# Kernel optimization log

Measured on AMD Instinct MI355X. Metric: run time of the kernel, lower is better.

## Reference

```python
import jax, jax.numpy as jnp
import numpy as np

BN_EPS = 1e-5

def _square_distance(src, dst):
    # src [B,N,3], dst [B,S,3] -> [B,N,S]
    d = -2.0 * jnp.einsum('bnc,bsc->bns', src, dst)
    d = d + jnp.sum(src * src, -1)[:, :, None]
    d = d + jnp.sum(dst * dst, -1)[:, None, :]
    return d

def _conv_bn_relu(x, w, b, g, beta):
    # x [B,C,N]; 1x1 conv == channel GEMM, then training-mode batchnorm over (B,N)
    y = jnp.einsum('oc,bcn->bon', w, x) + b[None, :, None]
    mean = jnp.mean(y, axis=(0, 2), keepdims=True)
    var = jnp.mean((y - mean) ** 2, axis=(0, 2), keepdims=True)  # biased, as torch BN uses for normalization
    y = (y - mean) * jax.lax.rsqrt(var + BN_EPS)
    y = y * g[None, :, None] + beta[None, :, None]
    return jax.nn.relu(y)

def setup_inputs() -> dict:
    key = jax.random.key(0)
    ks = jax.random.split(key, 8)
    B, N, S, D1, D2 = 8, 8192, 2048, 128, 256
    C_in, C_mid, C_out = D1 + D2, 256, 256
    return {
        'xyz1': jax.random.normal(ks[0], (B, 3, N), jnp.float32),
        'xyz2': jax.random.normal(ks[1], (B, 3, S), jnp.float32),
        'points1': jax.random.normal(ks[2], (B, D1, N), jnp.float32),
        'points2': jax.random.normal(ks[3], (B, D2, S), jnp.float32),
        'w1': jax.random.normal(ks[4], (C_mid, C_in), jnp.float32) * (1.0 / np.sqrt(C_in)),
        'b1': jax.random.normal(ks[5], (C_mid,), jnp.float32) * 0.01,
        'g1': jnp.ones((C_mid,), jnp.float32),
        'beta1': jnp.zeros((C_mid,), jnp.float32),
        'w2': jax.random.normal(ks[6], (C_out, C_mid), jnp.float32) * (1.0 / np.sqrt(C_mid)),
        'b2': jax.random.normal(ks[7], (C_out,), jnp.float32) * 0.01,
        'g2': jnp.ones((C_out,), jnp.float32),
        'beta2': jnp.zeros((C_out,), jnp.float32),
    }

def reference(xyz1, xyz2, points1, points2, w1, b1, g1, beta1, w2, b2, g2, beta2):
    B = xyz1.shape[0]
    p1xyz = jnp.transpose(xyz1, (0, 2, 1))      # [B,N,3]
    p2xyz = jnp.transpose(xyz2, (0, 2, 1))      # [B,S,3]
    p2 = jnp.transpose(points2, (0, 2, 1))      # [B,S,D2]

    dists = _square_distance(p1xyz, p2xyz)      # [B,N,S]
    neg_d3, idx = jax.lax.top_k(-dists, 3)      # 3 smallest distances
    d3 = -neg_d3                                # [B,N,3]
    recip = 1.0 / (d3 + 1e-8)
    weight = recip / jnp.sum(recip, axis=2, keepdims=True)  # [B,N,3]

    gathered = jax.vmap(lambda p, i: p[i])(p2, idx)          # [B,N,3,D2]
    interp = jnp.sum(gathered * weight[..., None], axis=2)   # [B,N,D2]

    new_points = jnp.concatenate([jnp.transpose(points1, (0, 2, 1)), interp], axis=-1)
    x = jnp.transpose(new_points, (0, 2, 1))    # [B,D1+D2,N]
    x = _conv_bn_relu(x, w1, b1, g1, beta1)
    x = _conv_bn_relu(x, w2, b2, g2, beta2)
    return x
```

## Files before the change

### kernel.cpp

```cpp
#include <hip/hip_runtime.h>

#define B_    8
#define N_    8192
#define S_    2048
#define D1_   128
#define D2_   256
#define CIN_  384
#define CMID_ 256
#define COUT_ 256

typedef unsigned int  u32;
typedef unsigned short u16;
typedef __attribute__((ext_vector_type(8))) short short8;
typedef __attribute__((ext_vector_type(4))) float f32x4;

static __device__ __forceinline__ u32 uminu(u32 a, u32 b) { return a < b ? a : b; }
static __device__ __forceinline__ u32 umaxu(u32 a, u32 b) { return a > b ? a : b; }
static __device__ __forceinline__ u32 umed3(u32 a, u32 b, u32 c) {
  u32 d;
  asm("v_med3_u32 %0, %1, %2, %3" : "=v"(d) : "v"(a), "v"(b), "v"(c));
  return d;
}
static __device__ __forceinline__ u16 f2bf(float f) {
  union { float f; u32 u; } v; v.f = f;
  u32 r = v.u + 0x7FFFu + ((v.u >> 16) & 1u);
  return (u16)(r >> 16);
}
static __device__ __forceinline__ float bflo(u32 u) { return __uint_as_float(u << 16); }
static __device__ __forceinline__ float bfhi(u32 u) { return __uint_as_float(u & 0xFFFF0000u); }
static __device__ __forceinline__ u32 cvtpk_bf16(float lo, float hi) {
  u32 d;
  asm("v_cvt_pk_bf16_f32 %0, %1, %2" : "=v"(d) : "v"(lo), "v"(hi));
  return d;
}

#define GLD16(g, l)                                                             \
  __builtin_amdgcn_global_load_lds((const __attribute__((address_space(1))) void*)(g), \
                                   (__attribute__((address_space(3))) void*)(l), 16, 0, 0)

__global__ __launch_bounds__(256) void k_pre(const float* __restrict__ xyz2,
                                             float4* __restrict__ pts4,
                                             const float* __restrict__ w1,
                                             const float* __restrict__ w2,
                                             u16* __restrict__ w1b,
                                             u16* __restrict__ w2b) {
  const int i = blockIdx.x * 256 + threadIdx.x;
  if (i < B_ * S_) {
    const int b = i >> 11, s = i & (S_ - 1);
    const float* xb = xyz2 + (size_t)b * 3 * S_;
    float x = xb[s], y = xb[S_ + s], z = xb[2 * S_ + s];
    pts4[b * S_ + s] = make_float4(-2.f * x, -2.f * y, -2.f * z, x * x + y * y + z * z);
    return;
  }
  const int j = i - B_ * S_;
  if (j < CMID_ * CIN_) { w1b[j] = f2bf(w1[j]); return; }
  const int h = j - CMID_ * CIN_;
  if (h < COUT_ * CMID_) w2b[h] = f2bf(w2[h]);
}

__global__ __launch_bounds__(256) void k_nn_scan(const float* __restrict__ xyz1,
                                                 const float4* __restrict__ pts4,
                                                 uint4* __restrict__ keys) {
  const int b = blockIdx.z, chunk = blockIdx.y;
  const int n = blockIdx.x * 256 + threadIdx.x;
  const float* pb = xyz1 + (size_t)b * 3 * N_;
  const float px = pb[n], py = pb[N_ + n], pz = pb[2 * N_ + n];
  const float pn = px * px + py * py + pz * pz;
  const float4* __restrict__ P = pts4 + b * S_ + chunk * 256;
  u32 m0 = ~0u, m1 = ~0u, m2 = ~0u;
#pragma unroll 8
  for (int s = 0; s < 256; ++s) {
    float4 q = P[s];
    float d = fmaf(px, q.x, fmaf(py, q.y, fmaf(pz, q.z, pn + q.w)));
    d = fmaxf(d, 0.f);
    u32 k = (__float_as_uint(d) & 0xFFFFFF00u) | (u32)s;
    u32 t = umaxu(m1, k);
    m1 = umed3(m0, m1, k);
    m2 = uminu(m2, t);
    m0 = uminu(m0, k);
  }
  uint4 v; v.x = m0; v.y = m1; v.z = m2; v.w = m2;
  keys[((size_t)(b * 8 + chunk)) * N_ + n] = v;
}

__global__ __launch_bounds__(256) void k_refine(const float* __restrict__ xyz1,
                                                const float4* __restrict__ pts4,
                                                const uint4* __restrict__ keys,
                                                int4* __restrict__ idx4,
                                                float4* __restrict__ w4) {
  const int b = blockIdx.y, n = blockIdx.x * 256 + threadIdx.x;
  const float* pb = xyz1 + (size_t)b * 3 * N_;
  const double px = (double)pb[n], py = (double)pb[N_ + n], pz = (double)pb[2 * N_ + n];
  const double pn = px * px + py * py + pz * pz;
  double bd0 = 1e300, bd1 = 1e300, bd2 = 1e300;
  int bi0 = 1 << 30, bi1 = 1 << 30, bi2 = 1 << 30;
#pragma unroll
  for (int c = 0; c < 8; ++c) {
    uint4 kk = keys[((size_t)(b * 8 + c)) * N_ + n];
    u32 arr[3] = {kk.x, kk.y, kk.z};
#pragma unroll
    for (int j = 0; j < 3; ++j) {
      int s = c * 256 + (int)(arr[j] & 255u);
      float4 q = pts4[b * S_ + s];
      double x = (double)(q.x * -0.5f), y = (double)(q.y * -0.5f), z = (double)(q.z * -0.5f);
      double dot = px * x + py * y + pz * z;
      double d = -2.0 * dot + (pn + (x * x + y * y + z * z));
      if (d < bd2 || (d == bd2 && s < bi2)) {
        if (d < bd1 || (d == bd1 && s < bi1)) {
          bd2 = bd1; bi2 = bi1;
          if (d < bd0 || (d == bd0 && s < bi0)) { bd1 = bd0; bi1 = bi0; bd0 = d; bi0 = s; }
          else                                  { bd1 = d;  bi1 = s; }
        } else { bd2 = d; bi2 = s; }
      }
    }
  }
  float f0 = (float)bd0, f1 = (float)bd1, f2 = (float)bd2;
  float r0 = 1.f / (f0 + 1e-8f), r1 = 1.f / (f1 + 1e-8f), r2 = 1.f / (f2 + 1e-8f);
  float rs = r0 + r1 + r2;
  w4[(size_t)b * N_ + n]   = make_float4(r0 / rs, r1 / rs, r2 / rs, 0.f);
  idx4[(size_t)b * N_ + n] = make_int4(bi0, bi1, bi2, 0);
}

__global__ __launch_bounds__(256) void k_p2t(const float* __restrict__ p2,
                                             float* __restrict__ p2T) {
  __shared__ float t[32][33];
  const int b = blockIdx.z, s0 = blockIdx.x * 32, d0 = blockIdx.y * 32;
  const int cc = threadIdx.x & 31, rr = threadIdx.x >> 5;
#pragma unroll
  for (int i = 0; i < 4; ++i) {
    int r = rr + i * 8;
    t[r][cc] = p2[((size_t)b * D2_ + d0 + r) * S_ + s0 + cc];
  }
  __syncthreads();
#pragma unroll
  for (int i = 0; i < 4; ++i) {
    int r = rr + i * 8;
    p2T[((size_t)b * S_ + s0 + r) * D2_ + d0 + cc] = t[cc][r];
  }
}

__global__ __launch_bounds__(256) void k_packp1(const float* __restrict__ p1,
                                                u16* __restrict__ xT) {
  __shared__ float t[32][33];
  const int b = blockIdx.z, n0 = blockIdx.x * 32, c0 = blockIdx.y * 32;
  const int cc = threadIdx.x & 31, rr = threadIdx.x >> 5;
#pragma unroll
  for (int i = 0; i < 4; ++i) {
    int r = rr + i * 8;
    t[r][cc] = p1[((size_t)b * D1_ + c0 + r) * N_ + n0 + cc];
  }
  __syncthreads();
#pragma unroll
  for (int i = 0; i < 4; ++i) {
    int r = rr + i * 8;
    xT[((size_t)b * N_ + n0 + r) * CIN_ + c0 + cc] = f2bf(t[cc][r]);
  }
}

__global__ __launch_bounds__(256) void k_gather_pack(const float* __restrict__ p2T,
                                                     const int4* __restrict__ idx4,
                                                     const float4* __restrict__ w4,
                                                     u16* __restrict__ xT) {
  const int b = blockIdx.y;
  const int wv = threadIdx.x >> 6, lane = threadIdx.x & 63;
  const int nbase = blockIdx.x * 16 + wv * 4;
  int4   id[4];
  float4 w[4];
#pragma unroll
  for (int i = 0; i < 4; ++i) {
    id[i] = idx4[(size_t)b * N_ + nbase + i];
    w[i]  = w4[(size_t)b * N_ + nbase + i];
  }
#pragma unroll
  for (int i = 0; i < 4; ++i) {
    const int n = nbase + i;
    const float4* r0 = (const float4*)(p2T + ((size_t)b * S_ + id[i].x) * D2_) + lane;
    const float4* r1 = (const float4*)(p2T + ((size_t)b * S_ + id[i].y) * D2_) + lane;
    const float4* r2 = (const float4*)(p2T + ((size_t)b * S_ + id[i].z) * D2_) + lane;
    float4 a = *r0, bb = *r1, cq = *r2;
    ushort4 pk;
    pk.x = f2bf(a.x * w[i].x + bb.x * w[i].y + cq.x * w[i].z);
    pk.y = f2bf(a.y * w[i].x + bb.y * w[i].y + cq.y * w[i].z);
    pk.z = f2bf(a.z * w[i].x + bb.z * w[i].y + cq.z * w[i].z);
    pk.w = f2bf(a.w * w[i].x + bb.w * w[i].y + cq.w * w[i].z);
    *(ushort4*)(xT + ((size_t)b * N_ + n) * CIN_ + D1_ + lane * 4) = pk;
  }
}

__global__ __launch_bounds__(64) void k_bnstat(const float* __restrict__ ps,
                                               const float* __restrict__ pq,
                                               const float* __restrict__ g,
                                               const float* __restrict__ beta,
                                               float* __restrict__ scale,
                                               float* __restrict__ shift) {
  const int o = blockIdx.x, l = threadIdx.x;
  float s = 0.f, q = 0.f;
#pragma unroll
  for (int i = 0; i < 8; ++i) {
    s += ps[(size_t)o * 512 + i * 64 + l];
    q += pq[(size_t)o * 512 + i * 64 + l];
  }
#pragma unroll
  for (int m = 1; m <= 32; m <<= 1) { s += __shfl_xor(s, m); q += __shfl_xor(q, m); }
  if (l == 0) {
    const float inv = 1.0f / (float)(B_ * N_);
    float mean = s * inv;
    float var = q * inv - mean * mean;
    float sc = g[o] / sqrtf(var + 1e-5f);
    scale[o] = sc;
    shift[o] = beta[o] - mean * sc;
  }
}

__global__ __launch_bounds__(512) void k_gemm1(const u16* __restrict__ Wb,
                                               const float* __restrict__ bias,
                                               const u16* __restrict__ xT,
                                               u16* __restrict__ y1T,
                                               float* __restrict__ psum,
                                               float* __restrict__ pssq) {
  __shared__ u16 As[2][8192];
  __shared__ u16 Bs[2][4096];
  __shared__ float s_sum[256], s_ssq[256];
  const int b = blockIdx.z, bn0 = blockIdx.x * 128;
  const int tid = threadIdx.x, w = tid >> 6, l = tid & 63;
  const int wm = w & 3, wn = w >> 2;
  const int lr = l >> 2, lc = l & 3;
  const int fm = l & 15, fq = l >> 4;
  const int clog = (lc ^ ((lr >> 1) & 3)) * 8;
  const int swz8 = (fq ^ ((fm >> 1) & 3)) * 8;
  if (tid < 256) { s_sum[tid] = 0.f; s_ssq[tid] = 0.f; }
  f32x4 acc[4][4];
#pragma unroll
  for (int i = 0; i < 4; ++i)
#pragma unroll
    for (int j = 0; j < 4; ++j) acc[i][j] = (f32x4){0.f, 0.f, 0.f, 0.f};

  const int NK = CIN_ / 32;
#pragma unroll
  for (int j = 0; j < 2; ++j) {
    int seg = w * 2 + j, row = seg * 16 + lr;
    GLD16(Wb + (size_t)row * CIN_ + clog, &As[0][seg * 512]);
  }
  {
    int row = w * 16 + lr;
    GLD16(xT + ((size_t)b * N_ + bn0 + row) * CIN_ + clog, &Bs[0][w * 512]);
  }
  for (int kk = 0; kk < NK; ++kk) {
    __syncthreads();
    const int cur = kk & 1;
    if (kk + 1 < NK) {
      const int k0 = (kk + 1) * 32, nxt = cur ^ 1;
#pragma unroll
      for (int j = 0; j < 2; ++j) {
        int seg = w * 2 + j, row = seg * 16 + lr;
        GLD16(Wb + (size_t)row * CIN_ + k0 + clog, &As[nxt][seg * 512]);
      }
      int row = w * 16 + lr;
      GLD16(xT + ((size_t)b * N_ + bn0 + row) * CIN_ + k0 + clog, &Bs[nxt][w * 512]);
    }
    short8 af[4], bfr[4];
#pragma unroll
    for (int f = 0; f < 4; ++f) {
      af[f]  = *(const short8*)&As[cur][(wm * 64 + f * 16 + fm) * 32 + swz8];
      bfr[f] = *(const short8*)&Bs[cur][(wn * 64 + f * 16 + fm) * 32 + swz8];
    }
#pragma unroll
    for (int i = 0; i < 4; ++i)
#pragma unroll
      for (int j = 0; j < 4; ++j)
        acc[i][j] = __builtin_amdgcn_mfma_f32_16x16x32_bf16(af[i], bfr[j], acc[i][j], 0, 0, 0);
  }
  u16* tb = y1T + ((size_t)b * 64 + (bn0 >> 7)) * 32768;
#pragma unroll
  for (int i = 0; i < 4; ++i) {
    int ob = wm * 64 + i * 16 + fq * 4;
    float4 b4 = *(const float4*)(bias + ob);
    float sv0 = 0, sv1 = 0, sv2 = 0, sv3 = 0, qv0 = 0, qv1 = 0, qv2 = 0, qv3 = 0;
#pragma unroll
    for (int j = 0; j < 4; ++j) {
      int nl = wn * 64 + j * 16 + fm;
      ushort4 pk;
      pk.x = f2bf(acc[i][j][0] + b4.x);
      pk.y = f2bf(acc[i][j][1] + b4.y);
      pk.z = f2bf(acc[i][j][2] + b4.z);
      pk.w = f2bf(acc[i][j][3] + b4.w);
      *(ushort4*)(tb + (size_t)(ob >> 5) * 4096 + nl * 32 + (ob & 31)) = pk;
      float v0 = bflo(pk.x), v1 = bflo(pk.y), v2 = bflo(pk.z), v3 = bflo(pk.w);
      sv0 += v0; sv1 += v1; sv2 += v2; sv3 += v3;
      qv0 = fmaf(v0, v0, qv0); qv1 = fmaf(v1, v1, qv1);
      qv2 = fmaf(v2, v2, qv2); qv3 = fmaf(v3, v3, qv3);
    }
#pragma unroll
    for (int m = 1; m <= 8; m <<= 1) {
      sv0 += __shfl_xor(sv0, m); sv1 += __shfl_xor(sv1, m);
      sv2 += __shfl_xor(sv2, m); sv3 += __shfl_xor(sv3, m);
      qv0 += __shfl_xor(qv0, m); qv1 += __shfl_xor(qv1, m);
      qv2 += __shfl_xor(qv2, m); qv3 += __shfl_xor(qv3, m);
    }
    if (fm == 0) {
      atomicAdd(&s_sum[ob + 0], sv0); atomicAdd(&s_sum[ob + 1], sv1);
      atomicAdd(&s_sum[ob + 2], sv2); atomicAdd(&s_sum[ob + 3], sv3);
      atomicAdd(&s_ssq[ob + 0], qv0); atomicAdd(&s_ssq[ob + 1], qv1);
      atomicAdd(&s_ssq[ob + 2], qv2); atomicAdd(&s_ssq[ob + 3], qv3);
    }
  }
  __syncthreads();
  if (tid < 256) {
    const int blk = blockIdx.x + 64 * blockIdx.z;
    psum[(size_t)tid * 512 + blk] = s_sum[tid];
    pssq[(size_t)tid * 512 + blk] = s_ssq[tid];
  }
}

__global__ __launch_bounds__(512) void k_gemm2(const u16* __restrict__ Wb2,
                                               const float* __restrict__ b2,
                                               const u16* __restrict__ y1T,
                                               const float* __restrict__ scale,
                                               const float* __restrict__ shift,
                                               u16* __restrict__ y2T,
                                               float* __restrict__ psum,
                                               float* __restrict__ pssq) {
  __shared__ u16 As[2][8192];
  __shared__ u16 Bs[2][4096];
  __shared__ float s_sum[256], s_ssq[256];
  __shared__ float s_sc[CMID_], s_sh[CMID_];
  const int b = blockIdx.z, bn0 = blockIdx.x * 128;
  const int tid = threadIdx.x, w = tid >> 6, l = tid & 63;
  const int wm = w & 3, wn = w >> 2;
  const int lr = l >> 2, lc = l & 3;
  const int fm = l & 15, fq = l >> 4;
  const int clog = (lc ^ ((lr >> 1) & 3)) * 8;
  const int swz8 = (fq ^ ((fm >> 1) & 3)) * 8;
  if (tid < 256) {
    s_sum[tid] = 0.f; s_ssq[tid] = 0.f;
    s_sc[tid] = scale[tid];
    s_sh[tid] = shift[tid];
  }
  f32x4 acc[4][4];
#pragma unroll
  for (int i = 0; i < 4; ++i)
#pragma unroll
    for (int j = 0; j < 4; ++j) acc[i][j] = (f32x4){0.f, 0.f, 0.f, 0.f};

  const u16* tb = y1T + ((size_t)b * 64 + (bn0 >> 7)) * 32768;
  const int NK = CMID_ / 32;
#pragma unroll
  for (int j = 0; j < 2; ++j) {
    int seg = w * 2 + j, row = seg * 16 + lr;
    GLD16(Wb2 + (size_t)row * CMID_ + clog, &As[0][seg * 512]);
  }
  {
    int row = w * 16 + lr;
    GLD16(tb + row * 32 + clog, &Bs[0][w * 512]);
  }
  for (int kk = 0; kk < NK; ++kk) {
    __syncthreads();
    const int cur = kk & 1;
    if (kk + 1 < NK) {
      const int nxt = cur ^ 1;
#pragma unroll
      for (int j = 0; j < 2; ++j) {
        int seg = w * 2 + j, row = seg * 16 + lr;
        GLD16(Wb2 + (size_t)row * CMID_ + (kk + 1) * 32 + clog, &As[nxt][seg * 512]);
      }
      int row = w * 16 + lr;
      GLD16(tb + (size_t)(kk + 1) * 4096 + row * 32 + clog, &Bs[nxt][w * 512]);
    }
    const int kb = kk * 32 + fq * 8;
    float4 s0 = *(const float4*)&s_sc[kb], s1 = *(const float4*)&s_sc[kb + 4];
    float4 h0 = *(const float4*)&s_sh[kb], h1 = *(const float4*)&s_sh[kb + 4];
    short8 af[4], bfr[4];
#pragma unroll
    for (int f = 0; f < 4; ++f) {
      af[f] = *(const short8*)&As[cur][(wm * 64 + f * 16 + fm) * 32 + swz8];
      uint4 r = *(const uint4*)&Bs[cur][(wn * 64 + f * 16 + fm) * 32 + swz8];
      float v0 = fmaxf(fmaf(bflo(r.x), s0.x, h0.x), 0.f);
      float v1 = fmaxf(fmaf(bfhi(r.x), s0.y, h0.y), 0.f);
      float v2 = fmaxf(fmaf(bflo(r.y), s0.z, h0.z), 0.f);
      float v3 = fmaxf(fmaf(bfhi(r.y), s0.w, h0.w), 0.f);
      float v4 = fmaxf(fmaf(bflo(r.z), s1.x, h1.x), 0.f);
      float v5 = fmaxf(fmaf(bfhi(r.z), s1.y, h1.y), 0.f);
      float v6 = fmaxf(fmaf(bflo(r.w), s1.z, h1.z), 0.f);
      float v7 = fmaxf(fmaf(bfhi(r.w), s1.w, h1.w), 0.f);
      union { u32 u[4]; short8 s; } cv;
      cv.u[0] = cvtpk_bf16(v0, v1); cv.u[1] = cvtpk_bf16(v2, v3);
      cv.u[2] = cvtpk_bf16(v4, v5); cv.u[3] = cvtpk_bf16(v6, v7);
      bfr[f] = cv.s;
    }
#pragma unroll
    for (int i = 0; i < 4; ++i)
#pragma unroll
      for (int j = 0; j < 4; ++j)
        acc[i][j] = __builtin_amdgcn_mfma_f32_16x16x32_bf16(af[i], bfr[j], acc[i][j], 0, 0, 0);
  }
  u16* tb2 = y2T + ((size_t)b * 64 + (bn0 >> 7)) * 32768;
#pragma unroll
  for (int i = 0; i < 4; ++i) {
    int ob = wm * 64 + i * 16 + fq * 4;
    float4 b4 = *(const float4*)(b2 + ob);
    float sv0 = 0, sv1 = 0, sv2 = 0, sv3 = 0, qv0 = 0, qv1 = 0, qv2 = 0, qv3 = 0;
#pragma unroll
    for (int j = 0; j < 4; ++j) {
      int nl = wn * 64 + j * 16 + fm;
      ushort4 pk;
      pk.x = f2bf(acc[i][j][0] + b4.x);
      pk.y = f2bf(acc[i][j][1] + b4.y);
      pk.z = f2bf(acc[i][j][2] + b4.z);
      pk.w = f2bf(acc[i][j][3] + b4.w);
      *(ushort4*)(tb2 + (size_t)(ob >> 5) * 4096 + nl * 32 + (ob & 31)) = pk;
      float v0 = bflo(pk.x), v1 = bflo(pk.y), v2 = bflo(pk.z), v3 = bflo(pk.w);
      sv0 += v0; sv1 += v1; sv2 += v2; sv3 += v3;
      qv0 = fmaf(v0, v0, qv0); qv1 = fmaf(v1, v1, qv1);
      qv2 = fmaf(v2, v2, qv2); qv3 = fmaf(v3, v3, qv3);
    }
#pragma unroll
    for (int m = 1; m <= 8; m <<= 1) {
      sv0 += __shfl_xor(sv0, m); sv1 += __shfl_xor(sv1, m);
      sv2 += __shfl_xor(sv2, m); sv3 += __shfl_xor(sv3, m);
      qv0 += __shfl_xor(qv0, m); qv1 += __shfl_xor(qv1, m);
      qv2 += __shfl_xor(qv2, m); qv3 += __shfl_xor(qv3, m);
    }
    if (fm == 0) {
      atomicAdd(&s_sum[ob + 0], sv0); atomicAdd(&s_sum[ob + 1], sv1);
      atomicAdd(&s_sum[ob + 2], sv2); atomicAdd(&s_sum[ob + 3], sv3);
      atomicAdd(&s_ssq[ob + 0], qv0); atomicAdd(&s_ssq[ob + 1], qv1);
      atomicAdd(&s_ssq[ob + 2], qv2); atomicAdd(&s_ssq[ob + 3], qv3);
    }
  }
  __syncthreads();
  if (tid < 256) {
    const int blk = blockIdx.x + 64 * blockIdx.z;
    psum[(size_t)tid * 512 + blk] = s_sum[tid];
    pssq[(size_t)tid * 512 + blk] = s_ssq[tid];
  }
}

__global__ __launch_bounds__(256) void k_bn2t(const u16* __restrict__ y2T,
                                              const float* __restrict__ scale,
                                              const float* __restrict__ shift,
                                              float* __restrict__ out) {
  __shared__ float t[32][33];
  const int b = blockIdx.z, n0 = blockIdx.x * 32, o0 = blockIdx.y * 32;
  const int cc = threadIdx.x & 31, rr = threadIdx.x >> 5;
  const float sc = scale[o0 + cc], sh = shift[o0 + cc];
  const u16* tb = y2T + ((size_t)b * 64 + (n0 >> 7)) * 32768 +
                  (size_t)(o0 >> 5) * 4096 + (size_t)(n0 & 96) * 32;
#pragma unroll
  for (int i = 0; i < 4; ++i) {
    int r = rr + i * 8;
    float v = bflo((u32)tb[r * 32 + cc]);
    t[r][cc] = fmaxf(fmaf(v, sc, sh), 0.f);
  }
  __syncthreads();
#pragma unroll
  for (int i = 0; i < 4; ++i) {
    int r = rr + i * 8;
    out[((size_t)b * COUT_ + o0 + r) * N_ + n0 + cc] = t[cc][r];
  }
}

extern "C" void kernel_launch(void* const* d_in, const int* in_sizes, int n_in,
                              void* d_out, int out_size, void* d_ws, size_t ws_size,
                              hipStream_t stream) {
  const float* xyz1    = (const float*)d_in[0];
  const float* xyz2    = (const float*)d_in[1];
  const float* points1 = (const float*)d_in[2];
  const float* points2 = (const float*)d_in[3];
  const float* w1      = (const float*)d_in[4];
  const float* b1      = (const float*)d_in[5];
  const float* g1      = (const float*)d_in[6];
  const float* beta1   = (const float*)d_in[7];
  const float* w2      = (const float*)d_in[8];
  const float* b2      = (const float*)d_in[9];
  const float* g2      = (const float*)d_in[10];
  const float* beta2   = (const float*)d_in[11];
  float* out = (float*)d_out;

  char* ws = (char*)d_ws;
  size_t off = 0;
  u16*    xT    = (u16*)(ws + off);    off += (size_t)B_ * N_ * CIN_ * 2;
  u16*    y1T   = (u16*)(ws + off);    off += (size_t)B_ * N_ * CMID_ * 2;
  float*  p2T   = (float*)(ws + off);  off += (size_t)B_ * S_ * D2_ * 4;
  float4* pts4  = (float4*)(ws + off); off += (size_t)B_ * S_ * 16;
  uint4*  keys  = (uint4*)(ws + off);  off += (size_t)B_ * 8 * N_ * 16;
  int4*   idx4  = (int4*)(ws + off);   off += (size_t)B_ * N_ * 16;
  float4* w4    = (float4*)(ws + off); off += (size_t)B_ * N_ * 16;
  u16*    w1b   = (u16*)(ws + off);    off += (size_t)CMID_ * CIN_ * 2;
  u16*    w2b   = (u16*)(ws + off);    off += (size_t)COUT_ * CMID_ * 2;
  float*  stats = (float*)(ws + off);  off += 1024 * sizeof(float);
  u16*    y2T   = xT;
  float* psum1 = (float*)keys;
  float* pssq1 = psum1 + 256 * 512;
  float* psum2 = pssq1 + 256 * 512;
  float* pssq2 = psum2 + 256 * 512;
  float* scale1 = stats,        * shift1 = stats + 256;
  float* scale2 = stats + 512,  * shift2 = stats + 768;

  k_pre        <<<dim3((B_ * S_ + CMID_ * CIN_ + COUT_ * CMID_) / 256), 256, 0, stream>>>(
                   xyz2, pts4, w1, w2, w1b, w2b);
  k_p2t        <<<dim3(S_ / 32, D2_ / 32, B_), 256, 0, stream>>>(points2, p2T);
  k_nn_scan    <<<dim3(N_ / 256, 8, B_), 256, 0, stream>>>(xyz1, pts4, keys);
  k_refine     <<<dim3(N_ / 256, B_), 256, 0, stream>>>(xyz1, pts4, keys, idx4, w4);
  k_packp1     <<<dim3(N_ / 32, D1_ / 32, B_), 256, 0, stream>>>(points1, xT);
  k_gather_pack<<<dim3(N_ / 16, B_), 256, 0, stream>>>(p2T, idx4, w4, xT);
  k_gemm1      <<<dim3(N_ / 128, 1, B_), 512, 0, stream>>>(w1b, b1, xT, y1T,
                                                           psum1, pssq1);
  k_bnstat     <<<dim3(CMID_), 64, 0, stream>>>(psum1, pssq1, g1, beta1, scale1, shift1);
  k_gemm2      <<<dim3(N_ / 128, 1, B_), 512, 0, stream>>>(w2b, b2, y1T,
                                                           scale1, shift1,
                                                           y2T, psum2, pssq2);
  k_bnstat     <<<dim3(COUT_), 64, 0, stream>>>(psum2, pssq2, g2, beta2, scale2, shift2);
  k_bn2t       <<<dim3(N_ / 32, COUT_ / 32, B_), 256, 0, stream>>>(y2T, scale2, shift2, out);
}
```

Baseline: 271.2 us.

## Triple-buffer GEMM LDS pipeline with explicit waitcnt barriers and coalesced BN partials

Both GEMM kernels move from double to triple buffering in LDS. Loads are issued two k-steps ahead, and each iteration waits with an explicit vmcnt and a single s_barrier instead of __syncthreads, so global-to-LDS loads overlap more with the MFMA work. The BN partial-sum layout is transposed to [blk][channel] so the per-block stores are coalesced, at the cost of strided reads in k_bnstat. The top-3 scan also replaces its max/min update with a single med3 instruction. LDS use per block grows, which may reduce occupancy.

```diff
diff --git a/kernel.cpp b/kernel.cpp
--- a/kernel.cpp
+++ b/kernel.cpp
@@ -15,7 +15,6 @@
 typedef __attribute__((ext_vector_type(4))) float f32x4;
 
 static __device__ __forceinline__ u32 uminu(u32 a, u32 b) { return a < b ? a : b; }
-static __device__ __forceinline__ u32 umaxu(u32 a, u32 b) { return a > b ? a : b; }
 static __device__ __forceinline__ u32 umed3(u32 a, u32 b, u32 c) {
   u32 d;
   asm("v_med3_u32 %0, %1, %2, %3" : "=v"(d) : "v"(a), "v"(b), "v"(c));
@@ -37,6 +36,12 @@
 #define GLD16(g, l)                                                             \
   __builtin_amdgcn_global_load_lds((const __attribute__((address_space(1))) void*)(g), \
                                    (__attribute__((address_space(3))) void*)(l), 16, 0, 0)
+
+#define WB(N)                                                                   \
+  __builtin_amdgcn_sched_barrier(0);                                            \
+  asm volatile("s_waitcnt vmcnt(" #N ")" ::: "memory");                         \
+  __builtin_amdgcn_s_barrier();                                                 \
+  __builtin_amdgcn_sched_barrier(0);
 
 __global__ __launch_bounds__(256) void k_pre(const float* __restrict__ xyz2,
                                              float4* __restrict__ pts4,
@@ -74,10 +79,10 @@
     float d = fmaf(px, q.x, fmaf(py, q.y, fmaf(pz, q.z, pn + q.w)));
     d = fmaxf(d, 0.f);
     u32 k = (__float_as_uint(d) & 0xFFFFFF00u) | (u32)s;
-    u32 t = umaxu(m1, k);
+    u32 m2n = umed3(m1, m2, k);
     m1 = umed3(m0, m1, k);
-    m2 = uminu(m2, t);
     m0 = uminu(m0, k);
+    m2 = m2n;
   }
   uint4 v; v.x = m0; v.y = m1; v.z = m2; v.w = m2;
   keys[((size_t)(b * 8 + chunk)) * N_ + n] = v;
@@ -197,8 +202,8 @@
   float s = 0.f, q = 0.f;
 #pragma unroll
   for (int i = 0; i < 8; ++i) {
-    s += ps[(size_t)o * 512 + i * 64 + l];
-    q += pq[(size_t)o * 512 + i * 64 + l];
+    s += ps[(size_t)(i * 64 + l) * 256 + o];
+    q += pq[(size_t)(i * 64 + l) * 256 + o];
   }
 #pragma unroll
   for (int m = 1; m <= 32; m <<= 1) { s += __shfl_xor(s, m); q += __shfl_xor(q, m); }
@@ -218,8 +223,8 @@
                                                u16* __restrict__ y1T,
                                                float* __restrict__ psum,
                                                float* __restrict__ pssq) {
-  __shared__ u16 As[2][8192];
-  __shared__ u16 Bs[2][4096];
+  __shared__ u16 As[3][8192];
+  __shared__ u16 Bs[3][4096];
   __shared__ float s_sum[256], s_ssq[256];
   const int b = blockIdx.z, bn0 = blockIdx.x * 128;
   const int tid = threadIdx.x, w = tid >> 6, l = tid & 63;
@@ -228,7 +233,6 @@
   const int fm = l & 15, fq = l >> 4;
   const int clog = (lc ^ ((lr >> 1) & 3)) * 8;
   const int swz8 = (fq ^ ((fm >> 1) & 3)) * 8;
-  if (tid < 256) { s_sum[tid] = 0.f; s_ssq[tid] = 0.f; }
   f32x4 acc[4][4];
 #pragma unroll
   for (int i = 0; i < 4; ++i)
@@ -236,27 +240,27 @@
     for (int j = 0; j < 4; ++j) acc[i][j] = (f32x4){0.f, 0.f, 0.f, 0.f};
 
   const int NK = CIN_ / 32;
-#pragma unroll
-  for (int j = 0; j < 2; ++j) {
-    int seg = w * 2 + j, row = seg * 16 + lr;
-    GLD16(Wb + (size_t)row * CIN_ + clog, &As[0][seg * 512]);
-  }
-  {
-    int row = w * 16 + lr;
-    GLD16(xT + ((size_t)b * N_ + bn0 + row) * CIN_ + clog, &Bs[0][w * 512]);
-  }
+
+#define STAGE1(kk, buf)                                                         \
+  {                                                                             \
+    const int k0_ = (kk) * 32;                                                  \
+    _Pragma("unroll") for (int j_ = 0; j_ < 2; ++j_) {                          \
+      int seg_ = w * 2 + j_, row_ = seg_ * 16 + lr;                             \
+      GLD16(Wb + (size_t)row_ * CIN_ + k0_ + clog, &As[buf][seg_ * 512]);       \
+    }                                                                           \
+    int brow_ = w * 16 + lr;                                                    \
+    GLD16(xT + ((size_t)b * N_ + bn0 + brow_) * CIN_ + k0_ + clog,              \
+          &Bs[buf][w * 512]);                                                   \
+  }
+
+  STAGE1(0, 0);
+  STAGE1(1, 1);
+  int cur = 0;
   for (int kk = 0; kk < NK; ++kk) {
-    __syncthreads();
-    const int cur = kk & 1;
-    if (kk + 1 < NK) {
-      const int k0 = (kk + 1) * 32, nxt = cur ^ 1;
-#pragma unroll
-      for (int j = 0; j < 2; ++j) {
-        int seg = w * 2 + j, row = seg * 16 + lr;
-        GLD16(Wb + (size_t)row * CIN_ + k0 + clog, &As[nxt][seg * 512]);
-      }
-      int row = w * 16 + lr;
-      GLD16(xT + ((size_t)b * N_ + bn0 + row) * CIN_ + k0 + clog, &Bs[nxt][w * 512]);
+    if (kk + 1 < NK) { WB(3) } else { WB(0) }
+    if (kk + 2 < NK) {
+      int bt = cur + 2; if (bt >= 3) bt -= 3;
+      STAGE1(kk + 2, bt);
     }
     short8 af[4], bfr[4];
 #pragma unroll
@@ -269,7 +273,12 @@
 #pragma unroll
       for (int j = 0; j < 4; ++j)
         acc[i][j] = __builtin_amdgcn_mfma_f32_16x16x32_bf16(af[i], bfr[j], acc[i][j], 0, 0, 0);
-  }
+    ++cur; if (cur == 3) cur = 0;
+  }
+#undef STAGE1
+
+  if (tid < 256) { s_sum[tid] = 0.f; s_ssq[tid] = 0.f; }
+  __syncthreads();
   u16* tb = y1T + ((size_t)b * 64 + (bn0 >> 7)) * 32768;
 #pragma unroll
   for (int i = 0; i < 4; ++i) {
@@ -307,8 +316,8 @@
   __syncthreads();
   if (tid < 256) {
     const int blk = blockIdx.x + 64 * blockIdx.z;
-    psum[(size_t)tid * 512 + blk] = s_sum[tid];
-    pssq[(size_t)tid * 512 + blk] = s_ssq[tid];
+    psum[(size_t)blk * 256 + tid] = s_sum[tid];
+    pssq[(size_t)blk * 256 + tid] = s_ssq[tid];
   }
 }
 
@@ -320,8 +329,8 @@
                                                u16* __restrict__ y2T,
                                                float* __restrict__ psum,
                                                float* __restrict__ pssq) {
-  __shared__ u16 As[2][8192];
-  __shared__ u16 Bs[2][4096];
+  __shared__ u16 As[3][8192];
+  __shared__ u16 Bs[3][4096];
   __shared__ float s_sum[256], s_ssq[256];
   __shared__ float s_sc[CMID_], s_sh[CMID_];
   const int b = blockIdx.z, bn0 = blockIdx.x * 128;
@@ -332,7 +341,6 @@
   const int clog = (lc ^ ((lr >> 1) & 3)) * 8;
   const int swz8 = (fq ^ ((fm >> 1) & 3)) * 8;
   if (tid < 256) {
-    s_sum[tid] = 0.f; s_ssq[tid] = 0.f;
     s_sc[tid] = scale[tid];
     s_sh[tid] = shift[tid];
   }
@@ -344,27 +352,26 @@
 
   const u16* tb = y1T + ((size_t)b * 64 + (bn0 >> 7)) * 32768;
   const int NK = CMID_ / 32;
-#pragma unroll
-  for (int j = 0; j < 2; ++j) {
-    int seg = w * 2 + j, row = seg * 16 + lr;
-    GLD16(Wb2 + (size_t)row * CMID_ + clog, &As[0][seg * 512]);
-  }
-  {
-    int row = w * 16 + lr;
-    GLD16(tb + row * 32 + clog, &Bs[0][w * 512]);
-  }
+
+#define STAGE2(kk, buf)                                                         \
+  {                                                                             \
+    const int k0_ = (kk) * 32;                                                  \
+    _Pragma("unroll") for (int j_ = 0; j_ < 2; ++j_) {                          \
+      int seg_ = w * 2 + j_, row_ = seg_ * 16 + lr;                             \
+      GLD16(Wb2 + (size_t)row_ * CMID_ + k0_ + clog, &As[buf][seg_ * 512]);     \
+    }                                                                           \
+    int brow_ = w * 16 + lr;                                                    \
+    GLD16(tb + (size_t)(kk) * 4096 + brow_ * 32 + clog, &Bs[buf][w * 512]);     \
+  }
+
+  STAGE2(0, 0);
+  STAGE2(1, 1);
+  int cur = 0;
   for (int kk = 0; kk < NK; ++kk) {
-    __syncthreads();
-    const int cur = kk & 1;
-    if (kk + 1 < NK) {
-      const int nxt = cur ^ 1;
-#pragma unroll
-      for (int j = 0; j < 2; ++j) {
-        int seg = w * 2 + j, row = seg * 16 + lr;
-        GLD16(Wb2 + (size_t)row * CMID_ + (kk + 1) * 32 + clog, &As[nxt][seg * 512]);
-      }
-      int row = w * 16 + lr;
-      GLD16(tb + (size_t)(kk + 1) * 4096 + row * 32 + clog, &Bs[nxt][w * 512]);
+    if (kk + 1 < NK) { WB(3) } else { WB(0) }
+    if (kk + 2 < NK) {
+      int bt = cur + 2; if (bt >= 3) bt -= 3;
+      STAGE2(kk + 2, bt);
     }
     const int kb = kk * 32 + fq * 8;
     float4 s0 = *(const float4*)&s_sc[kb], s1 = *(const float4*)&s_sc[kb + 4];
@@ -392,7 +399,12 @@
 #pragma unroll
       for (int j = 0; j < 4; ++j)
         acc[i][j] = __builtin_amdgcn_mfma_f32_16x16x32_bf16(af[i], bfr[j], acc[i][j], 0, 0, 0);
-  }
+    ++cur; if (cur == 3) cur = 0;
+  }
+#undef STAGE2
+
+  if (tid < 256) { s_sum[tid] = 0.f; s_ssq[tid] = 0.f; }
+  __syncthreads();
   u16* tb2 = y2T + ((size_t)b * 64 + (bn0 >> 7)) * 32768;
 #pragma unroll
   for (int i = 0; i < 4; ++i) {
@@ -430,8 +442,8 @@
   __syncthreads();
   if (tid < 256) {
     const int blk = blockIdx.x + 64 * blockIdx.z;
-    psum[(size_t)tid * 512 + blk] = s_sum[tid];
-    pssq[(size_t)tid * 512 + blk] = s_ssq[tid];
+    psum[(size_t)blk * 256 + tid] = s_sum[tid];
+    pssq[(size_t)blk * 256 + tid] = s_ssq[tid];
   }
 }
 
```

After: 273.4 us. No clear change (+0.8%).
